# Kernel tuning notes

Hardware: AMD Instinct MI355X
Metric: run time of the kernel (lower is better)

## Reference

```python
import jax, jax.numpy as jnp
from jax import lax
import numpy as np

B, NW, L, E, H, V = 8192, 4, 16, 128, 128, 64  # batch, words/example, max chars, emsize, hidden, char vocab


def setup_inputs() -> dict:
    key = jax.random.key(0)
    ks = jax.random.split(key, 13)
    s = 0.05
    return {
        "word_ids": jax.random.randint(ks[0], (B, NW, L), 0, V, dtype=jnp.int32),
        "lengths": jax.random.randint(ks[1], (B, NW), 1, L + 1, dtype=jnp.int32),
        "emb_i": jax.random.normal(ks[2], (V, E), jnp.float32),
        "W_ih": jax.random.normal(ks[3], (4 * H, E), jnp.float32) * s,
        "W_hh": jax.random.normal(ks[4], (4 * H, H), jnp.float32) * s,
        "b_ih": jax.random.normal(ks[5], (4 * H,), jnp.float32) * s,
        "b_hh": jax.random.normal(ks[6], (4 * H,), jnp.float32) * s,
        "conv1_w": jax.random.normal(ks[7], (4, 1, 2, 2), jnp.float32) * 0.5,
        "conv1_b": jax.random.normal(ks[8], (4,), jnp.float32) * 0.1,
        "conv2_w": jax.random.normal(ks[9], (8, 4, 2, 2), jnp.float32) * 0.5,
        "conv2_b": jax.random.normal(ks[10], (8,), jnp.float32) * 0.1,
        "scorer_w": jax.random.normal(ks[11], (1, 2 * 2 * 8), jnp.float32) * 0.2,
        "scorer_b": jax.random.normal(ks[12], (1,), jnp.float32) * 0.1,
    }


def reference(word_ids, lengths, emb_i, W_ih, W_hh, b_ih, b_hh,
              conv1_w, conv1_b, conv2_w, conv2_b, scorer_w, scorer_b):
    Bx, NWx, Lx = word_ids.shape
    Hh = W_hh.shape[1]
    BN = Bx * NWx
    # char embeddings for all words, packed: [L, BN, E]
    xs = emb_i[word_ids.reshape(BN, Lx)].transpose(1, 0, 2)
    # ragged lengths -> per-step update mask [L, BN]
    mask = jnp.arange(Lx, dtype=lengths.dtype)[:, None] < lengths.reshape(-1)[None, :]
    h0 = jnp.zeros((BN, Hh), emb_i.dtype)

    def step(carry, xm):
        h, c = carry
        x_t, m = xm
        gates = x_t @ W_ih.T + b_ih + h @ W_hh.T + b_hh  # torch LSTMCell gate order i,f,g,o
        i, f, g, o = jnp.split(gates, 4, axis=-1)
        i = jax.nn.sigmoid(i); f = jax.nn.sigmoid(f)
        g = jnp.tanh(g); o = jax.nn.sigmoid(o)
        c_new = f * c + i * g
        h_new = o * jnp.tanh(c_new)
        m = m[:, None]
        return (jnp.where(m, h_new, h), jnp.where(m, c_new, c)), None

    (h, c), _ = lax.scan(step, (h0, h0), (xs, mask))
    # Model.encode returns the cell state c
    reps = c.reshape(Bx, NWx, Hh)

    # pairwise cosine similarity matrix [B, NW, NW]
    norms = jnp.sqrt(jnp.sum(reps * reps, axis=-1))
    dots = jnp.einsum('bih,bjh->bij', reps, reps)
    cos = dots / (norms[:, :, None] * norms[:, None, :])

    # tiny 2-layer CNN scorer on the NWxNW matrix (NCHW)
    dn = ('NCHW', 'OIHW', 'NCHW')
    x_img = cos[:, None, :, :]
    out = jax.nn.relu(lax.conv_general_dilated(x_img, conv1_w, (1, 1), 'VALID', dimension_numbers=dn)
                      + conv1_b[None, :, None, None])
    out = jax.nn.relu(lax.conv_general_dilated(out, conv2_w, (1, 1), 'VALID', dimension_numbers=dn)
                      + conv2_b[None, :, None, None])
    flat = out.reshape(Bx, -1)  # channel-major flatten matches torch .view
    score = flat @ scorer_w.T + scorer_b
    return jax.nn.sigmoid(score)  # [B, 1] discriminator prob
```

## Files before the change

### kernel.cpp

```cpp
#include <hip/hip_runtime.h>

#define BSZ    8192
#define NWRD   4
#define SEQL   16
#define HDIM   128
#define VOCAB  64
#define NSEQ   (BSZ * NWRD)
#define WGSEQ  32
#define UPB    80
#define BINCAP (UPB * WGSEQ)
#define NBLK   512

#define AS1 __attribute__((address_space(1)))
#define AS3 __attribute__((address_space(3)))

typedef float    f32x4  __attribute__((ext_vector_type(4)));
typedef float    f32x16 __attribute__((ext_vector_type(16)));
typedef __bf16   bf16x8 __attribute__((ext_vector_type(8)));
typedef _Float16 f16x8  __attribute__((ext_vector_type(8)));
typedef int      i32x4  __attribute__((ext_vector_type(4)));

union AccU { f32x16 v; f32x4 q[4]; float f[16]; };

__device__ __forceinline__ unsigned short f2bf(float f) {
    unsigned int u = __builtin_bit_cast(unsigned int, f);
    return (unsigned short)((u + 0x7fff + ((u >> 16) & 1)) >> 16);
}
__device__ __forceinline__ float sigm(float x) {
    return __builtin_amdgcn_rcpf(1.f + __builtin_amdgcn_exp2f(x * -1.44269504f));
}

__global__ void prep4(const float* __restrict__ emb, const float* __restrict__ W_ih,
                      const float* __restrict__ b_ih, const float* __restrict__ b_hh,
                      const float* __restrict__ W_hh, const int* __restrict__ lengths,
                      unsigned short* __restrict__ P2H, unsigned short* __restrict__ WA,
                      int* __restrict__ perm, int* __restrict__ gh)
{
    __shared__ int lh[16], gbase[16];
    const int blk = blockIdx.x, tid = threadIdx.x;

    if (blk < 128) {
        int idx = blk * 256 + tid;
        int v = idx >> 9, g = (idx >> 7) & 3, j = idx & 127;
        int n = g * 128 + j;
        const f32x4* er = (const f32x4*)(emb  + v * 128);
        const f32x4* wr = (const f32x4*)(W_ih + n * 128);
        f32x4 s4 = er[0] * wr[0];
#pragma unroll
        for (int e = 1; e < 32; ++e) s4 += er[e] * wr[e];
        float s = s4.x + s4.y + s4.z + s4.w + b_ih[n] + b_hh[n];
        int wv = j >> 5, jr = j & 31;
        int d = jr & 3, hl = (jr >> 2) & 1, q = jr >> 3;
        int cc = g * 16 + wv * 4 + hl * 2 + (q >> 1);
        int F  = v * 512 + ((cc ^ (v & 7)) << 3) + (q & 1) * 4 + d;
        P2H[F] = __builtin_bit_cast(unsigned short, (_Float16)s);
    } else if (blk < 384) {
        int idx = (blk - 128) * 256 + tid;
        int jj = idx & 7, lane = (idx >> 3) & 63, kc = (idx >> 9) & 7, tt = idx >> 12;
        int wv = tt >> 2, g = tt & 3;
        int n = g * 128 + wv * 32 + (lane & 31);
        int k = kc * 16 + (lane >> 5) * 8 + jj;
        WA[idx] = f2bf(W_hh[n * 128 + k]);
    } else {
        if (tid < 16) lh[tid] = 0;
        __syncthreads();
        int i = (blk - 384) * 256 + tid;
        int b = 16 - lengths[i];
        int rank = atomicAdd(&lh[b], 1);
        __syncthreads();
        if (tid < 16) gbase[tid] = atomicAdd(&gh[tid], lh[tid]);
        __syncthreads();
        perm[b * BINCAP + gbase[b] + rank] = i;
    }
}

__global__ __launch_bounds__(256, 2) void lstm4(
    const int* __restrict__ word_ids, const int* __restrict__ perm,
    int* __restrict__ gh, const unsigned short* __restrict__ P2H,
    const unsigned short* __restrict__ WA, float* __restrict__ c_out)
{
    __shared__ __align__(16) unsigned short ptab[VOCAB * 512];
    __shared__ __align__(16) unsigned short hbuf[2][WGSEQ * 128];

    const int tid    = threadIdx.x;
    const int wv     = tid >> 6;
    const int lane   = tid & 63;
    const int lane31 = lane & 31;
    const int hl     = lane >> 5;

    {
        const char* src = (const char*)P2H;
        char*       dst = (char*)ptab;
#pragma unroll
        for (int r = 0; r < 16; ++r) {
            const int off = r * 4096 + wv * 1024;
            __builtin_amdgcn_global_load_lds(
                (const AS1 unsigned int*)(src + off + lane * 16),
                (AS3 unsigned int*)(dst + off), 16, 0, 0);
        }
    }

    bf16x8 afr[4][8];
#pragma unroll
    for (int g = 0; g < 4; ++g)
#pragma unroll
        for (int kc = 0; kc < 8; ++kc)
            afr[g][kc] = *(const bf16x8*)(WA + (((wv * 4 + g) * 8 + kc) * 64 + lane) * 8);

    int ghs[16];
#pragma unroll
    for (int i = 0; i < 16; ++i)
        ghs[i] = __builtin_amdgcn_readfirstlane(gh[i]);
    int tot = 0;
#pragma unroll
    for (int i = 0; i < 16; ++i) tot += (ghs[i] + 31) >> 5;

    const int      rdo_b = lane31 * 256;
    const unsigned xv    = (unsigned)((lane31 & 7) << 4);
    const int      jbase = wv * 32 + 4 * hl;
    const int      ccb   = wv * 4 + hl * 2;
    int* const tick_p = (int*)&hbuf[0][0];

    for (;;) {
        __syncthreads();
        if (tid == 0) *tick_p = atomicAdd(gh + 16, 1);
        __syncthreads();
        const int k = *tick_p;
        if (k >= tot) break;

        int rem = k, bsel = 0, found = 0;
#pragma unroll
        for (int b2 = 0; b2 < 16; ++b2) {
            int nb = (ghs[b2] + 31) >> 5;
            if (!found) {
                if (rem < nb) { bsel = b2; found = 1; }
                else rem -= nb;
            }
        }
        const int widx = rem;
        const int cnt  = ghs[bsel];
        const int ml   = 16 - bsel;

        const int slot = widx * WGSEQ + lane31;
        const int live = slot < cnt;
        const int sid  = live ? perm[bsel * BINCAP + slot] : 0;
        unsigned long long u0, u1;
        {
            const i32x4* wp = (const i32x4*)(word_ids + sid * SEQL);
            i32x4 a = wp[0], b4 = wp[1], c4 = wp[2], d4 = wp[3];
            unsigned lo0 = (unsigned)(a.x  | (a.y  << 8) | (a.z  << 16) | (a.w  << 24));
            unsigned hi0 = (unsigned)(b4.x | (b4.y << 8) | (b4.z << 16) | (b4.w << 24));
            unsigned lo1 = (unsigned)(c4.x | (c4.y << 8) | (c4.z << 16) | (c4.w << 24));
            unsigned hi1 = (unsigned)(d4.x | (d4.y << 8) | (d4.z << 16) | (d4.w << 24));
            u0 = ((unsigned long long)hi0 << 32) | lo0;
            u1 = ((unsigned long long)hi1 << 32) | lo1;
        }

        f32x4 cq[4] = {{0,0,0,0},{0,0,0,0},{0,0,0,0},{0,0,0,0}};

#pragma unroll 1
        for (int t = 0; t < ml; ++t) {
            const int w = (int)(u0 & 63);
            u0 = (u0 >> 8) | (u1 << 56); u1 >>= 8;

            AccU acc[4];
            {
                const char*    rowp = (const char*)ptab + (w << 10);
                const unsigned wx   = (unsigned)((w & 7) << 4);
#pragma unroll
                for (int g = 0; g < 4; ++g)
#pragma unroll
                    for (int s = 0; s < 2; ++s) {
                        const unsigned off =
                            ((unsigned)((g * 16 + ccb + s) << 4)) ^ wx;
                        f16x8 hv = *(const f16x8*)(rowp + off);
#pragma unroll
                        for (int kk = 0; kk < 8; ++kk)
                            acc[g].f[s * 8 + kk] = (float)hv[kk];
                    }
            }

            if (t > 0) {
                const char* hr = (const char*)hbuf[t & 1];
                bf16x8 bfv[8];
#pragma unroll
                for (int kc = 0; kc < 8; ++kc)
                    bfv[kc] = *(const bf16x8*)(hr + rdo_b +
                                  (((unsigned)(kc * 32 + hl * 16)) ^ xv));
#pragma unroll
                for (int kc = 0; kc < 8; ++kc) {
                    const bf16x8 bb = bfv[kc];
#pragma unroll
                    for (int g = 0; g < 4; ++g)
                        acc[g].v = __builtin_amdgcn_mfma_f32_32x32x16_bf16(
                            afr[g][kc], bb, acc[g].v, 0, 0, 0);
                }
            }

            const int wr = (t < ml - 1);
            char* hw = (char*)hbuf[(t + 1) & 1];
#pragma unroll
            for (int q = 0; q < 4; ++q) {
                float hv4[4];
#pragma unroll
                for (int d = 0; d < 4; ++d) {
                    const int r = q * 4 + d;
                    float ei = __builtin_amdgcn_exp2f(acc[0].f[r] * -1.44269504f);
                    float ef = __builtin_amdgcn_exp2f(acc[1].f[r] * -1.44269504f);
                    float eg = __builtin_amdgcn_exp2f(acc[2].f[r] *  2.88539008f);
                    float ai = 1.f + ei, af = 1.f + ef, ag = 1.f + eg;
                    float t1 = ai * ag;
                    float R  = __builtin_amdgcn_rcpf(t1 * af);
                    float cn = __builtin_fmaf(cq[q][d], t1, (eg - 1.f) * af) * R;
                    cq[q][d] = cn;
                    if (wr) {
                        float eo = __builtin_amdgcn_exp2f(acc[3].f[r] * -1.44269504f);
                        float ec = __builtin_amdgcn_exp2f(cn * 2.88539008f);
                        hv4[d] = (ec - 1.f) *
                                 __builtin_amdgcn_rcpf((1.f + eo) * (1.f + ec));
                    }
                }
                if (wr) {
                    unsigned int plo_, phi_;
                    asm("v_cvt_pk_bf16_f32 %0, %1, %2"
                        : "=v"(plo_) : "v"(hv4[0]), "v"(hv4[1]));
                    asm("v_cvt_pk_bf16_f32 %0, %1, %2"
                        : "=v"(phi_) : "v"(hv4[2]), "v"(hv4[3]));
                    unsigned long long pu_ =
                        ((unsigned long long)phi_ << 32) | plo_;
                    *(unsigned long long*)(hw + rdo_b +
                        (((unsigned)(wv * 64 + q * 16)) ^ xv) + hl * 8) = pu_;
                }
            }
            if (wr) __syncthreads();
        }

        if (live) {
#pragma unroll
            for (int q = 0; q < 4; ++q)
                *(f32x4*)(c_out + sid * HDIM + jbase + 8 * q) = cq[q];
        }
    }
}

__global__ __launch_bounds__(256) void epilogue(
    const float* __restrict__ c_ws,
    const float* __restrict__ conv1_w, const float* __restrict__ conv1_b,
    const float* __restrict__ conv2_w, const float* __restrict__ conv2_b,
    const float* __restrict__ scorer_w, const float* __restrict__ scorer_b,
    float* __restrict__ out)
{
    __shared__ __align__(16) float reps[8 * NWRD * HDIM];
    __shared__ float gram_s[8 * 16];

    const int tid = threadIdx.x;
    const int b0  = blockIdx.x * 8;

    for (int i = tid; i < 8 * NWRD * HDIM; i += 256)
        reps[i] = c_ws[b0 * NWRD * HDIM + i];
    __syncthreads();

    const int bt  = tid >> 5;
    const int sub = tid & 31;

    float dval = 0.f;
    if (sub < 16) {
        int i = sub >> 2, j = sub & 3;
        const f32x4* ci = (const f32x4*)(reps + (bt * 4 + i) * HDIM);
        const f32x4* cj = (const f32x4*)(reps + (bt * 4 + j) * HDIM);
        f32x4 s4 = {0.f, 0.f, 0.f, 0.f};
        for (int k = 0; k < HDIM / 4; ++k) s4 += ci[k] * cj[k];
        dval = s4.x + s4.y + s4.z + s4.w;
        gram_s[bt * 16 + sub] = dval;
    }
    __syncthreads();
    float cosv = 0.f;
    if (sub < 16) {
        int i = sub >> 2, j = sub & 3;
        float di = gram_s[bt * 16 + i * 4 + i];
        float dj = gram_s[bt * 16 + j * 4 + j];
        cosv = __fdividef(dval, sqrtf(di * dj));
    }
    __syncthreads();
    if (sub < 16) gram_s[bt * 16 + sub] = cosv;
    __syncthreads();

    if (sub == 0) {
        float img[4][4];
#pragma unroll
        for (int i = 0; i < 4; ++i)
#pragma unroll
            for (int j = 0; j < 4; ++j) img[i][j] = gram_s[bt * 16 + i * 4 + j];

        float o1[4][3][3];
#pragma unroll
        for (int ch = 0; ch < 4; ++ch) {
            float w00 = conv1_w[ch*4+0], w01 = conv1_w[ch*4+1];
            float w10 = conv1_w[ch*4+2], w11 = conv1_w[ch*4+3];
            float bb  = conv1_b[ch];
#pragma unroll
            for (int y = 0; y < 3; ++y)
#pragma unroll
                for (int x = 0; x < 3; ++x) {
                    float s = bb + w00*img[y][x]   + w01*img[y][x+1]
                                 + w10*img[y+1][x] + w11*img[y+1][x+1];
                    o1[ch][y][x] = s > 0.f ? s : 0.f;
                }
        }
        float sc = scorer_b[0];
#pragma unroll
        for (int oc = 0; oc < 8; ++oc) {
            float bb = conv2_b[oc];
#pragma unroll
            for (int y = 0; y < 2; ++y)
#pragma unroll
                for (int x = 0; x < 2; ++x) {
                    float s = bb;
#pragma unroll
                    for (int ic = 0; ic < 4; ++ic) {
                        const float* w = conv2_w + oc * 16 + ic * 4;
                        s += w[0]*o1[ic][y][x]   + w[1]*o1[ic][y][x+1]
                           + w[2]*o1[ic][y+1][x] + w[3]*o1[ic][y+1][x+1];
                    }
                    float rl = s > 0.f ? s : 0.f;
                    sc += rl * scorer_w[oc * 4 + y * 2 + x];
                }
        }
        out[blockIdx.x * 8 + bt] = sigm(sc);
    }
}

extern "C" void kernel_launch(void* const* d_in, const int* in_sizes, int n_in,
                              void* d_out, int out_size, void* d_ws, size_t ws_size,
                              hipStream_t stream)
{
    const int*   word_ids = (const int*)d_in[0];
    const int*   lengths  = (const int*)d_in[1];
    const float* emb      = (const float*)d_in[2];
    const float* W_ih     = (const float*)d_in[3];
    const float* W_hh     = (const float*)d_in[4];
    const float* b_ih     = (const float*)d_in[5];
    const float* b_hh     = (const float*)d_in[6];
    const float* conv1_w  = (const float*)d_in[7];
    const float* conv1_b  = (const float*)d_in[8];
    const float* conv2_w  = (const float*)d_in[9];
    const float* conv2_b  = (const float*)d_in[10];
    const float* scorer_w = (const float*)d_in[11];
    const float* scorer_b = (const float*)d_in[12];
    float* out = (float*)d_out;

    char* ws = (char*)d_ws;
    unsigned short* P2H  = (unsigned short*)(ws + 0);
    unsigned short* WA   = (unsigned short*)(ws + (128<<10));
    int*            perm = (int*)(ws + (256<<10));
    int*            gh   = (int*)(ws + (416<<10));
    float*          c_ws = (float*)(ws + (512<<10));

    hipMemsetAsync(gh, 0, 17 * sizeof(int), stream);
    prep4   <<<512,  256, 0, stream>>>(emb, W_ih, b_ih, b_hh, W_hh, lengths,
                                       P2H, WA, perm, gh);
    lstm4   <<<NBLK, 256, 0, stream>>>(word_ids, perm, gh, P2H, WA, c_ws);
    epilogue<<<BSZ / 8, 256, 0, stream>>>(c_ws, conv1_w, conv1_b, conv2_w, conv2_b,
                                          scorer_w, scorer_b, out);
}
```

Before: 167.9 us.

## Fuse prep, LSTM and epilogue into one persistent kernel with grid barriers

Replaces the three kernel launches (prep, LSTM, epilogue) with a single persistent kernel of NBLK workgroups. The phases are separated by a software grid barrier built on atomics in the workspace. The goal is to remove launch gaps and kernel-boundary drains. The cost is the barrier spin, and all 512 blocks must be co-resident or the kernel deadlocks. The epilogue now processes two groups per block and reuses LDS.

```diff
diff --git a/kernel.cpp b/kernel.cpp
--- a/kernel.cpp
+++ b/kernel.cpp
@@ -30,13 +30,41 @@
     return __builtin_amdgcn_rcpf(1.f + __builtin_amdgcn_exp2f(x * -1.44269504f));
 }
 
-__global__ void prep4(const float* __restrict__ emb, const float* __restrict__ W_ih,
-                      const float* __restrict__ b_ih, const float* __restrict__ b_hh,
-                      const float* __restrict__ W_hh, const int* __restrict__ lengths,
-                      unsigned short* __restrict__ P2H, unsigned short* __restrict__ WA,
-                      int* __restrict__ perm, int* __restrict__ gh)
+__device__ __forceinline__ void grid_barrier(int* bar, int* gen) {
+    __syncthreads();
+    if (threadIdx.x == 0) {
+        __threadfence();
+        int g = __hip_atomic_load(gen, __ATOMIC_SEQ_CST, __HIP_MEMORY_SCOPE_AGENT);
+        if (__hip_atomic_fetch_add(bar, 1, __ATOMIC_SEQ_CST,
+                                   __HIP_MEMORY_SCOPE_AGENT) == NBLK - 1) {
+            __hip_atomic_store(bar, 0, __ATOMIC_SEQ_CST, __HIP_MEMORY_SCOPE_AGENT);
+            __hip_atomic_fetch_add(gen, 1, __ATOMIC_SEQ_CST,
+                                   __HIP_MEMORY_SCOPE_AGENT);
+        } else {
+            while (__hip_atomic_load(gen, __ATOMIC_SEQ_CST,
+                                     __HIP_MEMORY_SCOPE_AGENT) == g)
+                __builtin_amdgcn_s_sleep(8);
+        }
+        __threadfence();
+    }
+    __syncthreads();
+}
+
+__global__ __launch_bounds__(256, 2) void fused(
+    const int* __restrict__ word_ids, const int* __restrict__ lengths,
+    const float* __restrict__ emb, const float* __restrict__ W_ih,
+    const float* __restrict__ W_hh, const float* __restrict__ b_ih,
+    const float* __restrict__ b_hh,
+    const float* __restrict__ conv1_w, const float* __restrict__ conv1_b,
+    const float* __restrict__ conv2_w, const float* __restrict__ conv2_b,
+    const float* __restrict__ scorer_w, const float* __restrict__ scorer_b,
+    unsigned short* __restrict__ P2H, unsigned short* __restrict__ WA,
+    int* __restrict__ perm, int* __restrict__ gh,
+    float* __restrict__ c_ws, float* __restrict__ out)
 {
-    __shared__ int lh[16], gbase[16];
+    __shared__ __align__(16) unsigned short ptab[VOCAB * 512];
+    __shared__ __align__(16) unsigned short hbuf[2][WGSEQ * 128];
+
     const int blk = blockIdx.x, tid = threadIdx.x;
 
     if (blk < 128) {
@@ -49,19 +77,21 @@
 #pragma unroll
         for (int e = 1; e < 32; ++e) s4 += er[e] * wr[e];
         float s = s4.x + s4.y + s4.z + s4.w + b_ih[n] + b_hh[n];
-        int wv = j >> 5, jr = j & 31;
-        int d = jr & 3, hl = (jr >> 2) & 1, q = jr >> 3;
-        int cc = g * 16 + wv * 4 + hl * 2 + (q >> 1);
+        int wv2 = j >> 5, jr = j & 31;
+        int d = jr & 3, hl2 = (jr >> 2) & 1, q = jr >> 3;
+        int cc = g * 16 + wv2 * 4 + hl2 * 2 + (q >> 1);
         int F  = v * 512 + ((cc ^ (v & 7)) << 3) + (q & 1) * 4 + d;
         P2H[F] = __builtin_bit_cast(unsigned short, (_Float16)s);
     } else if (blk < 384) {
         int idx = (blk - 128) * 256 + tid;
-        int jj = idx & 7, lane = (idx >> 3) & 63, kc = (idx >> 9) & 7, tt = idx >> 12;
-        int wv = tt >> 2, g = tt & 3;
-        int n = g * 128 + wv * 32 + (lane & 31);
-        int k = kc * 16 + (lane >> 5) * 8 + jj;
+        int jj = idx & 7, ln = (idx >> 3) & 63, kc = (idx >> 9) & 7, tt = idx >> 12;
+        int wv2 = tt >> 2, g = tt & 3;
+        int n = g * 128 + wv2 * 32 + (ln & 31);
+        int k = kc * 16 + (ln >> 5) * 8 + jj;
         WA[idx] = f2bf(W_hh[n * 128 + k]);
     } else {
+        int* lh    = (int*)&hbuf[0][0];
+        int* gbase = lh + 16;
         if (tid < 16) lh[tid] = 0;
         __syncthreads();
         int i = (blk - 384) * 256 + tid;
@@ -72,261 +102,254 @@
         __syncthreads();
         perm[b * BINCAP + gbase[b] + rank] = i;
     }
-}
-
-__global__ __launch_bounds__(256, 2) void lstm4(
-    const int* __restrict__ word_ids, const int* __restrict__ perm,
-    int* __restrict__ gh, const unsigned short* __restrict__ P2H,
-    const unsigned short* __restrict__ WA, float* __restrict__ c_out)
-{
-    __shared__ __align__(16) unsigned short ptab[VOCAB * 512];
-    __shared__ __align__(16) unsigned short hbuf[2][WGSEQ * 128];
-
-    const int tid    = threadIdx.x;
-    const int wv     = tid >> 6;
-    const int lane   = tid & 63;
-    const int lane31 = lane & 31;
-    const int hl     = lane >> 5;
+
+    grid_barrier(gh + 17, gh + 18);
 
     {
-        const char* src = (const char*)P2H;
-        char*       dst = (char*)ptab;
-#pragma unroll
-        for (int r = 0; r < 16; ++r) {
-            const int off = r * 4096 + wv * 1024;
-            __builtin_amdgcn_global_load_lds(
-                (const AS1 unsigned int*)(src + off + lane * 16),
-                (AS3 unsigned int*)(dst + off), 16, 0, 0);
+        const int wv     = tid >> 6;
+        const int lane   = tid & 63;
+        const int lane31 = lane & 31;
+        const int hl     = lane >> 5;
+
+        {
+            const char* src = (const char*)P2H;
+            char*       dst = (char*)ptab;
+#pragma unroll
+            for (int r = 0; r < 16; ++r) {
+                const int off = r * 4096 + wv * 1024;
+                __builtin_amdgcn_global_load_lds(
+                    (const AS1 unsigned int*)(src + off + lane * 16),
+                    (AS3 unsigned int*)(dst + off), 16, 0, 0);
+            }
+        }
+
+        bf16x8 afr[4][8];
+#pragma unroll
+        for (int g = 0; g < 4; ++g)
+#pragma unroll
+            for (int kc = 0; kc < 8; ++kc)
+                afr[g][kc] = *(const bf16x8*)(WA + (((wv * 4 + g) * 8 + kc) * 64 + lane) * 8);
+
+        int ghs[16];
+#pragma unroll
+        for (int i = 0; i < 16; ++i)
+            ghs[i] = __builtin_amdgcn_readfirstlane(gh[i]);
+        int tot = 0;
+#pragma unroll
+        for (int i = 0; i < 16; ++i) tot += (ghs[i] + 31) >> 5;
+
+        const int      rdo_b = lane31 * 256;
+        const unsigned xv    = (unsigned)((lane31 & 7) << 4);
+        const int      jbase = wv * 32 + 4 * hl;
+        const int      ccb   = wv * 4 + hl * 2;
+        int* const tick_p = (int*)&hbuf[0][0];
+
+        for (;;) {
+            __syncthreads();
+            if (tid == 0) *tick_p = atomicAdd(gh + 16, 1);
+            __syncthreads();
+            const int k = *tick_p;
+            if (k >= tot) break;
+
+            int rem = k, bsel = 0, found = 0;
+#pragma unroll
+            for (int b2 = 0; b2 < 16; ++b2) {
+                int nb = (ghs[b2] + 31) >> 5;
+                if (!found) {
+                    if (rem < nb) { bsel = b2; found = 1; }
+                    else rem -= nb;
+                }
+            }
+            const int widx = rem;
+            const int cnt  = ghs[bsel];
+            const int ml   = 16 - bsel;
+
+            const int slot = widx * WGSEQ + lane31;
+            const int live = slot < cnt;
+            const int sid  = live ? perm[bsel * BINCAP + slot] : 0;
+            unsigned long long u0, u1;
+            {
+                const i32x4* wp = (const i32x4*)(word_ids + sid * SEQL);
+                i32x4 a = wp[0], b4 = wp[1], c4 = wp[2], d4 = wp[3];
+                unsigned lo0 = (unsigned)(a.x  | (a.y  << 8) | (a.z  << 16) | (a.w  << 24));
+                unsigned hi0 = (unsigned)(b4.x | (b4.y << 8) | (b4.z << 16) | (b4.w << 24));
+                unsigned lo1 = (unsigned)(c4.x | (c4.y << 8) | (c4.z << 16) | (c4.w << 24));
+                unsigned hi1 = (unsigned)(d4.x | (d4.y << 8) | (d4.z << 16) | (d4.w << 24));
+                u0 = ((unsigned long long)hi0 << 32) | lo0;
+                u1 = ((unsigned long long)hi1 << 32) | lo1;
+            }
+
+            f32x4 cq[4] = {{0,0,0,0},{0,0,0,0},{0,0,0,0},{0,0,0,0}};
+
+#pragma unroll 1
+            for (int t = 0; t < ml; ++t) {
+                const int w = (int)(u0 & 63);
+                u0 = (u0 >> 8) | (u1 << 56); u1 >>= 8;
+
+                AccU acc[4];
+                {
+                    const char*    rowp = (const char*)ptab + (w << 10);
+                    const unsigned wx   = (unsigned)((w & 7) << 4);
+#pragma unroll
+                    for (int g = 0; g < 4; ++g)
+#pragma unroll
+                        for (int s = 0; s < 2; ++s) {
+                            const unsigned off =
+                                ((unsigned)((g * 16 + ccb + s) << 4)) ^ wx;
+                            f16x8 hv = *(const f16x8*)(rowp + off);
+#pragma unroll
+                            for (int kk = 0; kk < 8; ++kk)
+                                acc[g].f[s * 8 + kk] = (float)hv[kk];
+                        }
+                }
+
+                if (t > 0) {
+                    const char* hr = (const char*)hbuf[t & 1];
+                    bf16x8 bfv[8];
+#pragma unroll
+                    for (int kc = 0; kc < 8; ++kc)
+                        bfv[kc] = *(const bf16x8*)(hr + rdo_b +
+                                      (((unsigned)(kc * 32 + hl * 16)) ^ xv));
+#pragma unroll
+                    for (int kc = 0; kc < 8; ++kc) {
+                        const bf16x8 bb = bfv[kc];
+#pragma unroll
+                        for (int g = 0; g < 4; ++g)
+                            acc[g].v = __builtin_amdgcn_mfma_f32_32x32x16_bf16(
+                                afr[g][kc], bb, acc[g].v, 0, 0, 0);
+                    }
+                }
+
+                const int wr = (t < ml - 1);
+                char* hw = (char*)hbuf[(t + 1) & 1];
+#pragma unroll
+                for (int q = 0; q < 4; ++q) {
+                    float hv4[4];
+#pragma unroll
+                    for (int d = 0; d < 4; ++d) {
+                        const int r = q * 4 + d;
+                        float ei = __builtin_amdgcn_exp2f(acc[0].f[r] * -1.44269504f);
+                        float ef = __builtin_amdgcn_exp2f(acc[1].f[r] * -1.44269504f);
+                        float eg = __builtin_amdgcn_exp2f(acc[2].f[r] *  2.88539008f);
+                        float ai = 1.f + ei, af = 1.f + ef, ag = 1.f + eg;
+                        float t1 = ai * ag;
+                        float R  = __builtin_amdgcn_rcpf(t1 * af);
+                        float cn = __builtin_fmaf(cq[q][d], t1, (eg - 1.f) * af) * R;
+                        cq[q][d] = cn;
+                        if (wr) {
+                            float eo = __builtin_amdgcn_exp2f(acc[3].f[r] * -1.44269504f);
+                            float ec = __builtin_amdgcn_exp2f(cn * 2.88539008f);
+                            hv4[d] = (ec - 1.f) *
+                                     __builtin_amdgcn_rcpf((1.f + eo) * (1.f + ec));
+                        }
+                    }
+                    if (wr) {
+                        unsigned int plo_, phi_;
+                        asm("v_cvt_pk_bf16_f32 %0, %1, %2"
+                            : "=v"(plo_) : "v"(hv4[0]), "v"(hv4[1]));
+                        asm("v_cvt_pk_bf16_f32 %0, %1, %2"
+                            : "=v"(phi_) : "v"(hv4[2]), "v"(hv4[3]));
+                        unsigned long long pu_ =
+                            ((unsigned long long)phi_ << 32) | plo_;
+                        *(unsigned long long*)(hw + rdo_b +
+                            (((unsigned)(wv * 64 + q * 16)) ^ xv) + hl * 8) = pu_;
+                    }
+                }
+                if (wr) __syncthreads();
+            }
+
+            if (live) {
+#pragma unroll
+                for (int q = 0; q < 4; ++q)
+                    *(f32x4*)(c_ws + sid * HDIM + jbase + 8 * q) = cq[q];
+            }
         }
     }
 
-    bf16x8 afr[4][8];
-#pragma unroll
-    for (int g = 0; g < 4; ++g)
-#pragma unroll
-        for (int kc = 0; kc < 8; ++kc)
-            afr[g][kc] = *(const bf16x8*)(WA + (((wv * 4 + g) * 8 + kc) * 64 + lane) * 8);
-
-    int ghs[16];
-#pragma unroll
-    for (int i = 0; i < 16; ++i)
-        ghs[i] = __builtin_amdgcn_readfirstlane(gh[i]);
-    int tot = 0;
-#pragma unroll
-    for (int i = 0; i < 16; ++i) tot += (ghs[i] + 31) >> 5;
-
-    const int      rdo_b = lane31 * 256;
-    const unsigned xv    = (unsigned)((lane31 & 7) << 4);
-    const int      jbase = wv * 32 + 4 * hl;
-    const int      ccb   = wv * 4 + hl * 2;
-    int* const tick_p = (int*)&hbuf[0][0];
-
-    for (;;) {
-        __syncthreads();
-        if (tid == 0) *tick_p = atomicAdd(gh + 16, 1);
-        __syncthreads();
-        const int k = *tick_p;
-        if (k >= tot) break;
-
-        int rem = k, bsel = 0, found = 0;
-#pragma unroll
-        for (int b2 = 0; b2 < 16; ++b2) {
-            int nb = (ghs[b2] + 31) >> 5;
-            if (!found) {
-                if (rem < nb) { bsel = b2; found = 1; }
-                else rem -= nb;
+    grid_barrier(gh + 17, gh + 18);
+
+    {
+        float* reps = (float*)&hbuf[0][0];
+        float* gram = (float*)&ptab[0];
+
+        const int bt  = tid >> 5;
+        const int sub = tid & 31;
+
+#pragma unroll 1
+        for (int g2 = 0; g2 < 2; ++g2) {
+            const int grp = blk * 2 + g2;
+            __syncthreads();
+
+            for (int i = tid; i < 8 * NWRD * HDIM; i += 256)
+                reps[i] = c_ws[grp * (8 * NWRD * HDIM) + i];
+            __syncthreads();
+
+            float dval = 0.f;
+            if (sub < 16) {
+                int i = sub >> 2, j = sub & 3;
+                const f32x4* ci = (const f32x4*)(reps + (bt * 4 + i) * HDIM);
+                const f32x4* cj = (const f32x4*)(reps + (bt * 4 + j) * HDIM);
+                f32x4 s4 = {0.f, 0.f, 0.f, 0.f};
+                for (int k = 0; k < HDIM / 4; ++k) s4 += ci[k] * cj[k];
+                dval = s4.x + s4.y + s4.z + s4.w;
+                gram[bt * 16 + sub] = dval;
+            }
+            __syncthreads();
+            float cosv = 0.f;
+            if (sub < 16) {
+                int i = sub >> 2, j = sub & 3;
+                float di = gram[bt * 16 + i * 4 + i];
+                float dj = gram[bt * 16 + j * 4 + j];
+                cosv = __fdividef(dval, sqrtf(di * dj));
+            }
+            __syncthreads();
+            if (sub < 16) gram[bt * 16 + sub] = cosv;
+            __syncthreads();
+
+            if (sub == 0) {
+                float img[4][4];
+#pragma unroll
+                for (int i = 0; i < 4; ++i)
+#pragma unroll
+                    for (int j = 0; j < 4; ++j) img[i][j] = gram[bt * 16 + i * 4 + j];
+
+                float o1[4][3][3];
+#pragma unroll
+                for (int ch = 0; ch < 4; ++ch) {
+                    float w00 = conv1_w[ch*4+0], w01 = conv1_w[ch*4+1];
+                    float w10 = conv1_w[ch*4+2], w11 = conv1_w[ch*4+3];
+                    float bb  = conv1_b[ch];
+#pragma unroll
+                    for (int y = 0; y < 3; ++y)
+#pragma unroll
+                        for (int x = 0; x < 3; ++x) {
+                            float s = bb + w00*img[y][x]   + w01*img[y][x+1]
+                                         + w10*img[y+1][x] + w11*img[y+1][x+1];
+                            o1[ch][y][x] = s > 0.f ? s : 0.f;
+                        }
+                }
+                float sc = scorer_b[0];
+#pragma unroll
+                for (int oc = 0; oc < 8; ++oc) {
+                    float bb = conv2_b[oc];
+#pragma unroll
+                    for (int y = 0; y < 2; ++y)
+#pragma unroll
+                        for (int x = 0; x < 2; ++x) {
+                            float s = bb;
+#pragma unroll
+                            for (int ic = 0; ic < 4; ++ic) {
+                                const float* w = conv2_w + oc * 16 + ic * 4;
+                                s += w[0]*o1[ic][y][x]   + w[1]*o1[ic][y][x+1]
+                                   + w[2]*o1[ic][y+1][x] + w[3]*o1[ic][y+1][x+1];
+                            }
+                            float rl = s > 0.f ? s : 0.f;
+                            sc += rl * scorer_w[oc * 4 + y * 2 + x];
+                        }
+                }
+                out[grp * 8 + bt] = sigm(sc);
             }
         }
-        const int widx = rem;
-        const int cnt  = ghs[bsel];
-        const int ml   = 16 - bsel;
-
-        const int slot = widx * WGSEQ + lane31;
-        const int live = slot < cnt;
-        const int sid  = live ? perm[bsel * BINCAP + slot] : 0;
-        unsigned long long u0, u1;
-        {
-            const i32x4* wp = (const i32x4*)(word_ids + sid * SEQL);
-            i32x4 a = wp[0], b4 = wp[1], c4 = wp[2], d4 = wp[3];
-            unsigned lo0 = (unsigned)(a.x  | (a.y  << 8) | (a.z  << 16) | (a.w  << 24));
-            unsigned hi0 = (unsigned)(b4.x | (b4.y << 8) | (b4.z << 16) | (b4.w << 24));
-            unsigned lo1 = (unsigned)(c4.x | (c4.y << 8) | (c4.z << 16) | (c4.w << 24));
-            unsigned hi1 = (unsigned)(d4.x | (d4.y << 8) | (d4.z << 16) | (d4.w << 24));
-            u0 = ((unsigned long long)hi0 << 32) | lo0;
-            u1 = ((unsigned long long)hi1 << 32) | lo1;
-        }
-
-        f32x4 cq[4] = {{0,0,0,0},{0,0,0,0},{0,0,0,0},{0,0,0,0}};
-
-#pragma unroll 1
-        for (int t = 0; t < ml; ++t) {
-            const int w = (int)(u0 & 63);
-            u0 = (u0 >> 8) | (u1 << 56); u1 >>= 8;
-
-            AccU acc[4];
-            {
-                const char*    rowp = (const char*)ptab + (w << 10);
-                const unsigned wx   = (unsigned)((w & 7) << 4);
-#pragma unroll
-                for (int g = 0; g < 4; ++g)
-#pragma unroll
-                    for (int s = 0; s < 2; ++s) {
-                        const unsigned off =
-                            ((unsigned)((g * 16 + ccb + s) << 4)) ^ wx;
-                        f16x8 hv = *(const f16x8*)(rowp + off);
-#pragma unroll
-                        for (int kk = 0; kk < 8; ++kk)
-                            acc[g].f[s * 8 + kk] = (float)hv[kk];
-                    }
-            }
-
-            if (t > 0) {
-                const char* hr = (const char*)hbuf[t & 1];
-                bf16x8 bfv[8];
-#pragma unroll
-                for (int kc = 0; kc < 8; ++kc)
-                    bfv[kc] = *(const bf16x8*)(hr + rdo_b +
-                                  (((unsigned)(kc * 32 + hl * 16)) ^ xv));
-#pragma unroll
-                for (int kc = 0; kc < 8; ++kc) {
-                    const bf16x8 bb = bfv[kc];
-#pragma unroll
-                    for (int g = 0; g < 4; ++g)
-                        acc[g].v = __builtin_amdgcn_mfma_f32_32x32x16_bf16(
-                            afr[g][kc], bb, acc[g].v, 0, 0, 0);
-                }
-            }
-
-            const int wr = (t < ml - 1);
-            char* hw = (char*)hbuf[(t + 1) & 1];
-#pragma unroll
-            for (int q = 0; q < 4; ++q) {
-                float hv4[4];
-#pragma unroll
-                for (int d = 0; d < 4; ++d) {
-                    const int r = q * 4 + d;
-                    float ei = __builtin_amdgcn_exp2f(acc[0].f[r] * -1.44269504f);
-                    float ef = __builtin_amdgcn_exp2f(acc[1].f[r] * -1.44269504f);
-                    float eg = __builtin_amdgcn_exp2f(acc[2].f[r] *  2.88539008f);
-                    float ai = 1.f + ei, af = 1.f + ef, ag = 1.f + eg;
-                    float t1 = ai * ag;
-                    float R  = __builtin_amdgcn_rcpf(t1 * af);
-                    float cn = __builtin_fmaf(cq[q][d], t1, (eg - 1.f) * af) * R;
-                    cq[q][d] = cn;
-                    if (wr) {
-                        float eo = __builtin_amdgcn_exp2f(acc[3].f[r] * -1.44269504f);
-                        float ec = __builtin_amdgcn_exp2f(cn * 2.88539008f);
-                        hv4[d] = (ec - 1.f) *
-                                 __builtin_amdgcn_rcpf((1.f + eo) * (1.f + ec));
-                    }
-                }
-                if (wr) {
-                    unsigned int plo_, phi_;
-                    asm("v_cvt_pk_bf16_f32 %0, %1, %2"
-                        : "=v"(plo_) : "v"(hv4[0]), "v"(hv4[1]));
-                    asm("v_cvt_pk_bf16_f32 %0, %1, %2"
-                        : "=v"(phi_) : "v"(hv4[2]), "v"(hv4[3]));
-                    unsigned long long pu_ =
-                        ((unsigned long long)phi_ << 32) | plo_;
-                    *(unsigned long long*)(hw + rdo_b +
-                        (((unsigned)(wv * 64 + q * 16)) ^ xv) + hl * 8) = pu_;
-                }
-            }
-            if (wr) __syncthreads();
-        }
-
-        if (live) {
-#pragma unroll
-            for (int q = 0; q < 4; ++q)
-                *(f32x4*)(c_out + sid * HDIM + jbase + 8 * q) = cq[q];
-        }
-    }
-}
-
-__global__ __launch_bounds__(256) void epilogue(
-    const float* __restrict__ c_ws,
-    const float* __restrict__ conv1_w, const float* __restrict__ conv1_b,
-    const float* __restrict__ conv2_w, const float* __restrict__ conv2_b,
-    const float* __restrict__ scorer_w, const float* __restrict__ scorer_b,
-    float* __restrict__ out)
-{
-    __shared__ __align__(16) float reps[8 * NWRD * HDIM];
-    __shared__ float gram_s[8 * 16];
-
-    const int tid = threadIdx.x;
-    const int b0  = blockIdx.x * 8;
-
-    for (int i = tid; i < 8 * NWRD * HDIM; i += 256)
-        reps[i] = c_ws[b0 * NWRD * HDIM + i];
-    __syncthreads();
-
-    const int bt  = tid >> 5;
-    const int sub = tid & 31;
-
-    float dval = 0.f;
-    if (sub < 16) {
-        int i = sub >> 2, j = sub & 3;
-        const f32x4* ci = (const f32x4*)(reps + (bt * 4 + i) * HDIM);
-        const f32x4* cj = (const f32x4*)(reps + (bt * 4 + j) * HDIM);
-        f32x4 s4 = {0.f, 0.f, 0.f, 0.f};
-        for (int k = 0; k < HDIM / 4; ++k) s4 += ci[k] * cj[k];
-        dval = s4.x + s4.y + s4.z + s4.w;
-        gram_s[bt * 16 + sub] = dval;
-    }
-    __syncthreads();
-    float cosv = 0.f;
-    if (sub < 16) {
-        int i = sub >> 2, j = sub & 3;
-        float di = gram_s[bt * 16 + i * 4 + i];
-        float dj = gram_s[bt * 16 + j * 4 + j];
-        cosv = __fdividef(dval, sqrtf(di * dj));
-    }
-    __syncthreads();
-    if (sub < 16) gram_s[bt * 16 + sub] = cosv;
-    __syncthreads();
-
-    if (sub == 0) {
-        float img[4][4];
-#pragma unroll
-        for (int i = 0; i < 4; ++i)
-#pragma unroll
-            for (int j = 0; j < 4; ++j) img[i][j] = gram_s[bt * 16 + i * 4 + j];
-
-        float o1[4][3][3];
-#pragma unroll
-        for (int ch = 0; ch < 4; ++ch) {
-            float w00 = conv1_w[ch*4+0], w01 = conv1_w[ch*4+1];
-            float w10 = conv1_w[ch*4+2], w11 = conv1_w[ch*4+3];
-            float bb  = conv1_b[ch];
-#pragma unroll
-            for (int y = 0; y < 3; ++y)
-#pragma unroll
-                for (int x = 0; x < 3; ++x) {
-                    float s = bb + w00*img[y][x]   + w01*img[y][x+1]
-                                 + w10*img[y+1][x] + w11*img[y+1][x+1];
-                    o1[ch][y][x] = s > 0.f ? s : 0.f;
-                }
-        }
-        float sc = scorer_b[0];
-#pragma unroll
-        for (int oc = 0; oc < 8; ++oc) {
-            float bb = conv2_b[oc];
-#pragma unroll
-            for (int y = 0; y < 2; ++y)
-#pragma unroll
-                for (int x = 0; x < 2; ++x) {
-                    float s = bb;
-#pragma unroll
-                    for (int ic = 0; ic < 4; ++ic) {
-                        const float* w = conv2_w + oc * 16 + ic * 4;
-                        s += w[0]*o1[ic][y][x]   + w[1]*o1[ic][y][x+1]
-                           + w[2]*o1[ic][y+1][x] + w[3]*o1[ic][y+1][x+1];
-                    }
-                    float rl = s > 0.f ? s : 0.f;
-                    sc += rl * scorer_w[oc * 4 + y * 2 + x];
-                }
-        }
-        out[blockIdx.x * 8 + bt] = sigm(sc);
     }
 }
 
@@ -356,10 +379,9 @@
     int*            gh   = (int*)(ws + (416<<10));
     float*          c_ws = (float*)(ws + (512<<10));
 
-    hipMemsetAsync(gh, 0, 17 * sizeof(int), stream);
-    prep4   <<<512,  256, 0, stream>>>(emb, W_ih, b_ih, b_hh, W_hh, lengths,
-                                       P2H, WA, perm, gh);
-    lstm4   <<<NBLK, 256, 0, stream>>>(word_ids, perm, gh, P2H, WA, c_ws);
-    epilogue<<<BSZ / 8, 256, 0, stream>>>(c_ws, conv1_w, conv1_b, conv2_w, conv2_b,
-                                          scorer_w, scorer_b, out);
-}
+    hipMemsetAsync(gh, 0, 20 * sizeof(int), stream);
+    fused<<<NBLK, 256, 0, stream>>>(word_ids, lengths, emb, W_ih, W_hh, b_ih, b_hh,
+                                    conv1_w, conv1_b, conv2_w, conv2_b,
+                                    scorer_w, scorer_b,
+                                    P2H, WA, perm, gh, c_ws, out);
+}
```

After: 366.7 us. 118% more time.

## Fuse cosine/CNN scorer epilogue into LSTM kernel via per-batch completion counters

Applied to the files above, without the earlier changes.

Removes the separate epilogue kernel launch. After each LSTM work group writes its cell states, it atomically increments a per-batch counter, and the group that completes the fourth word of a batch computes the Gram matrix, the cosine values, the convs and the sigmoid score in one wavefront using shuffles. This saves a kernel launch and a full pass over c_ws. In exchange it adds atomics, fences and a serial per-batch tail inside the LSTM blocks, and the memset grows to cover the counters.

```diff
diff --git a/kernel.cpp b/kernel.cpp
--- a/kernel.cpp
+++ b/kernel.cpp
@@ -76,8 +76,12 @@
 
 __global__ __launch_bounds__(256, 2) void lstm4(
     const int* __restrict__ word_ids, const int* __restrict__ perm,
-    int* __restrict__ gh, const unsigned short* __restrict__ P2H,
-    const unsigned short* __restrict__ WA, float* __restrict__ c_out)
+    int* __restrict__ gh, int* __restrict__ bcount,
+    const unsigned short* __restrict__ P2H, const unsigned short* __restrict__ WA,
+    const float* __restrict__ conv1_w, const float* __restrict__ conv1_b,
+    const float* __restrict__ conv2_w, const float* __restrict__ conv2_b,
+    const float* __restrict__ scorer_w, const float* __restrict__ scorer_b,
+    float* __restrict__ c_ws, float* __restrict__ out)
 {
     __shared__ __align__(16) unsigned short ptab[VOCAB * 512];
     __shared__ __align__(16) unsigned short hbuf[2][WGSEQ * 128];
@@ -238,95 +242,83 @@
         if (live) {
 #pragma unroll
             for (int q = 0; q < 4; ++q)
-                *(f32x4*)(c_out + sid * HDIM + jbase + 8 * q) = cq[q];
-        }
-    }
-}
-
-__global__ __launch_bounds__(256) void epilogue(
-    const float* __restrict__ c_ws,
-    const float* __restrict__ conv1_w, const float* __restrict__ conv1_b,
-    const float* __restrict__ conv2_w, const float* __restrict__ conv2_b,
-    const float* __restrict__ scorer_w, const float* __restrict__ scorer_b,
-    float* __restrict__ out)
-{
-    __shared__ __align__(16) float reps[8 * NWRD * HDIM];
-    __shared__ float gram_s[8 * 16];
-
-    const int tid = threadIdx.x;
-    const int b0  = blockIdx.x * 8;
-
-    for (int i = tid; i < 8 * NWRD * HDIM; i += 256)
-        reps[i] = c_ws[b0 * NWRD * HDIM + i];
-    __syncthreads();
-
-    const int bt  = tid >> 5;
-    const int sub = tid & 31;
-
-    float dval = 0.f;
-    if (sub < 16) {
-        int i = sub >> 2, j = sub & 3;
-        const f32x4* ci = (const f32x4*)(reps + (bt * 4 + i) * HDIM);
-        const f32x4* cj = (const f32x4*)(reps + (bt * 4 + j) * HDIM);
-        f32x4 s4 = {0.f, 0.f, 0.f, 0.f};
-        for (int k = 0; k < HDIM / 4; ++k) s4 += ci[k] * cj[k];
-        dval = s4.x + s4.y + s4.z + s4.w;
-        gram_s[bt * 16 + sub] = dval;
-    }
-    __syncthreads();
-    float cosv = 0.f;
-    if (sub < 16) {
-        int i = sub >> 2, j = sub & 3;
-        float di = gram_s[bt * 16 + i * 4 + i];
-        float dj = gram_s[bt * 16 + j * 4 + j];
-        cosv = __fdividef(dval, sqrtf(di * dj));
-    }
-    __syncthreads();
-    if (sub < 16) gram_s[bt * 16 + sub] = cosv;
-    __syncthreads();
-
-    if (sub == 0) {
-        float img[4][4];
-#pragma unroll
-        for (int i = 0; i < 4; ++i)
-#pragma unroll
-            for (int j = 0; j < 4; ++j) img[i][j] = gram_s[bt * 16 + i * 4 + j];
-
-        float o1[4][3][3];
-#pragma unroll
-        for (int ch = 0; ch < 4; ++ch) {
-            float w00 = conv1_w[ch*4+0], w01 = conv1_w[ch*4+1];
-            float w10 = conv1_w[ch*4+2], w11 = conv1_w[ch*4+3];
-            float bb  = conv1_b[ch];
-#pragma unroll
-            for (int y = 0; y < 3; ++y)
-#pragma unroll
-                for (int x = 0; x < 3; ++x) {
-                    float s = bb + w00*img[y][x]   + w01*img[y][x+1]
-                                 + w10*img[y+1][x] + w11*img[y+1][x+1];
-                    o1[ch][y][x] = s > 0.f ? s : 0.f;
+                *(f32x4*)(c_ws + sid * HDIM + jbase + 8 * q) = cq[q];
+        }
+
+        __threadfence();
+        __syncthreads();
+        if (wv == 0) {
+            int myb = -1;
+            if (lane < 32 && live &&
+                atomicAdd(&bcount[sid >> 2], 1) == 3)
+                myb = sid >> 2;
+            unsigned long long mask = __ballot(myb >= 0);
+            if (mask) {
+                __threadfence();
+                while (mask) {
+                    const int srcl = (int)__builtin_ctzll(mask);
+                    mask &= mask - 1;
+                    const int bat = __shfl(myb, srcl);
+                    const int p  = lane >> 2, pi = p >> 2, pj = p & 3;
+                    const f32x4* ci4 = (const f32x4*)(c_ws + (bat * 4 + pi) * HDIM
+                                                      + (lane & 3) * 32);
+                    const f32x4* cj4 = (const f32x4*)(c_ws + (bat * 4 + pj) * HDIM
+                                                      + (lane & 3) * 32);
+                    f32x4 s4 = ci4[0] * cj4[0];
+#pragma unroll
+                    for (int kk = 1; kk < 8; ++kk) s4 += ci4[kk] * cj4[kk];
+                    float dv = s4.x + s4.y + s4.z + s4.w;
+                    dv += __shfl_xor(dv, 1);
+                    dv += __shfl_xor(dv, 2);
+                    float dot16[16];
+#pragma unroll
+                    for (int pp = 0; pp < 16; ++pp)
+                        dot16[pp] = __shfl(dv, pp * 4);
+                    float img[4][4];
+#pragma unroll
+                    for (int a = 0; a < 4; ++a)
+#pragma unroll
+                        for (int b3 = 0; b3 < 4; ++b3)
+                            img[a][b3] = __fdividef(dot16[a * 4 + b3],
+                                          sqrtf(dot16[a * 5] * dot16[b3 * 5]));
+                    float o1[4][3][3];
+#pragma unroll
+                    for (int ch = 0; ch < 4; ++ch) {
+                        float w00 = conv1_w[ch*4+0], w01 = conv1_w[ch*4+1];
+                        float w10 = conv1_w[ch*4+2], w11 = conv1_w[ch*4+3];
+                        float bbv = conv1_b[ch];
+#pragma unroll
+                        for (int y = 0; y < 3; ++y)
+#pragma unroll
+                            for (int x = 0; x < 3; ++x) {
+                                float s = bbv + w00*img[y][x]   + w01*img[y][x+1]
+                                              + w10*img[y+1][x] + w11*img[y+1][x+1];
+                                o1[ch][y][x] = s > 0.f ? s : 0.f;
+                            }
+                    }
+                    float sc = scorer_b[0];
+#pragma unroll
+                    for (int oc = 0; oc < 8; ++oc) {
+                        float bbv = conv2_b[oc];
+#pragma unroll
+                        for (int y = 0; y < 2; ++y)
+#pragma unroll
+                            for (int x = 0; x < 2; ++x) {
+                                float s = bbv;
+#pragma unroll
+                                for (int ic = 0; ic < 4; ++ic) {
+                                    const float* w = conv2_w + oc * 16 + ic * 4;
+                                    s += w[0]*o1[ic][y][x]   + w[1]*o1[ic][y][x+1]
+                                       + w[2]*o1[ic][y+1][x] + w[3]*o1[ic][y+1][x+1];
+                                }
+                                float rl = s > 0.f ? s : 0.f;
+                                sc += rl * scorer_w[oc * 4 + y * 2 + x];
+                            }
+                    }
+                    if (lane == 0) out[bat] = sigm(sc);
                 }
-        }
-        float sc = scorer_b[0];
-#pragma unroll
-        for (int oc = 0; oc < 8; ++oc) {
-            float bb = conv2_b[oc];
-#pragma unroll
-            for (int y = 0; y < 2; ++y)
-#pragma unroll
-                for (int x = 0; x < 2; ++x) {
-                    float s = bb;
-#pragma unroll
-                    for (int ic = 0; ic < 4; ++ic) {
-                        const float* w = conv2_w + oc * 16 + ic * 4;
-                        s += w[0]*o1[ic][y][x]   + w[1]*o1[ic][y][x+1]
-                           + w[2]*o1[ic][y+1][x] + w[3]*o1[ic][y+1][x+1];
-                    }
-                    float rl = s > 0.f ? s : 0.f;
-                    sc += rl * scorer_w[oc * 4 + y * 2 + x];
-                }
-        }
-        out[blockIdx.x * 8 + bt] = sigm(sc);
+            }
+        }
     }
 }
 
@@ -350,16 +342,17 @@
     float* out = (float*)d_out;
 
     char* ws = (char*)d_ws;
-    unsigned short* P2H  = (unsigned short*)(ws + 0);
-    unsigned short* WA   = (unsigned short*)(ws + (128<<10));
-    int*            perm = (int*)(ws + (256<<10));
-    int*            gh   = (int*)(ws + (416<<10));
-    float*          c_ws = (float*)(ws + (512<<10));
-
-    hipMemsetAsync(gh, 0, 17 * sizeof(int), stream);
-    prep4   <<<512,  256, 0, stream>>>(emb, W_ih, b_ih, b_hh, W_hh, lengths,
-                                       P2H, WA, perm, gh);
-    lstm4   <<<NBLK, 256, 0, stream>>>(word_ids, perm, gh, P2H, WA, c_ws);
-    epilogue<<<BSZ / 8, 256, 0, stream>>>(c_ws, conv1_w, conv1_b, conv2_w, conv2_b,
-                                          scorer_w, scorer_b, out);
-}
+    unsigned short* P2H    = (unsigned short*)(ws + 0);
+    unsigned short* WA     = (unsigned short*)(ws + (128<<10));
+    int*            perm   = (int*)(ws + (256<<10));
+    int*            gh     = (int*)(ws + (416<<10));
+    int*            bcount = gh + 32;
+    float*          c_ws   = (float*)(ws + (512<<10));
+
+    hipMemsetAsync(gh, 0, (32 + BSZ) * sizeof(int), stream);
+    prep4<<<512,  256, 0, stream>>>(emb, W_ih, b_ih, b_hh, W_hh, lengths,
+                                    P2H, WA, perm, gh);
+    lstm4<<<NBLK, 256, 0, stream>>>(word_ids, perm, gh, bcount, P2H, WA,
+                                    conv1_w, conv1_b, conv2_w, conv2_b,
+                                    scorer_w, scorer_b, c_ws, out);
+}
```

New measurement: 490.7 us. 2.92x slower.
